# Kernel optimization log

Measured on AMD Instinct MI355X. Metric: run time of the kernel, lower is better.

Reference implementation:

```python
import jax, jax.numpy as jnp
import numpy as np

D, T, F, H = 5, 8192, 768, 64


def setup_inputs() -> dict:
    key = jax.random.key(0)
    ks = jax.random.split(key, 30)
    s = 0.05
    rn = lambda k, shape: jax.random.normal(k, shape, dtype=jnp.float32) * s
    return {
        "text_input": jax.random.normal(ks[0], (1, D, T, F), dtype=jnp.float32),
        "time_inputs": jax.random.uniform(ks[1], (1, D, T), dtype=jnp.float32),
        "num_layer": 0,
        # TimeLSTM params (PyTorch Linear convention: W [out,in], y = x @ W.T + b)
        "W_all_w": rn(ks[2], (4 * H, H)), "W_all_b": rn(ks[3], (4 * H,)),
        "U_all_w": rn(ks[4], (4 * H, F)), "U_all_b": rn(ks[5], (4 * H,)),
        "W_d_w": rn(ks[6], (H, H)), "W_d_b": rn(ks[7], (H,)),
        # text attention
        "ta_W1_w": rn(ks[8], (H, H)), "ta_W1_b": rn(ks[9], (H,)),
        "ta_W2_w": rn(ks[10], (H, H)), "ta_W2_b": rn(ks[11], (H,)),
        "ta_V_w": rn(ks[12], (1, H)), "ta_V_b": rn(ks[13], (1,)),
        # day nn.LSTM(64,64) params, gate order i,f,g,o
        "lstm_Wih": rn(ks[14], (4 * H, H)), "lstm_Whh": rn(ks[15], (4 * H, H)),
        "lstm_bih": rn(ks[16], (4 * H,)), "lstm_bhh": rn(ks[17], (4 * H,)),
        # day attention
        "da_W1_w": rn(ks[18], (H, H)), "da_W1_b": rn(ks[19], (H,)),
        "da_W2_w": rn(ks[20], (H, H)), "da_W2_b": rn(ks[21], (H,)),
        "da_V_w": rn(ks[22], (1, H)), "da_V_b": rn(ks[23], (1,)),
        "stock_w": rn(ks[24], (1, H)), "stock_b": rn(ks[25], (1,)),
    }


def reference(text_input, time_inputs, num_layer,
              W_all_w, W_all_b, U_all_w, U_all_b, W_d_w, W_d_b,
              ta_W1_w, ta_W1_b, ta_W2_w, ta_W2_b, ta_V_w, ta_V_b,
              lstm_Wih, lstm_Whh, lstm_bih, lstm_bhh,
              da_W1_w, da_W1_b, da_W2_w, da_W2_b, da_V_w, da_V_b,
              stock_w, stock_b):
    x = text_input[0]      # [D, T, F] -- days are independent, vectorize over them
    ts = time_inputs[0]    # [D, T]
    d = x.shape[0]

    # Precompute the big input projection as one GEMM: [D,T,4H]
    ux = jnp.einsum('dtf,gf->dtg', x, U_all_w) + U_all_b
    ux_t = jnp.transpose(ux, (1, 0, 2))  # [T, D, 4H]
    ts_t = ts.T                          # [T, D]

    def step(carry, inp):
        h, c = carry
        u, t = inp
        c_s1 = jnp.tanh(c @ W_d_w.T + W_d_b)
        c_adj = c - c_s1 + c_s1 * t[:, None]
        outs = h @ W_all_w.T + W_all_b + u
        f, i, o, g = jnp.split(outs, 4, axis=1)  # TimeLSTM chunk order f,i,o,c_tmp
        f = jax.nn.sigmoid(f); i = jax.nn.sigmoid(i); o = jax.nn.sigmoid(o)
        c = f * c_adj + i * jnp.tanh(g)
        h = o * jnp.tanh(c)
        return (h, c), o  # original appends the (sigmoided) output gate

    h0 = jnp.zeros((d, H), x.dtype)
    (h_fin, _), outs = jax.lax.scan(step, (h0, h0), (ux_t, ts_t))
    y = jnp.tanh(jnp.transpose(outs, (1, 0, 2)))  # [D, T, H]

    # text attention: additive attention pooled over T, per day
    score = jnp.tanh((h_fin @ ta_W1_w.T + ta_W1_b)[:, None, :] + y @ ta_W2_w.T + ta_W2_b) @ ta_V_w.T + ta_V_b
    attn = jax.nn.softmax(score, axis=1)          # [D, T, 1]
    ctx = jnp.sum(attn * y, axis=1)               # [D, H]

    # day nn.LSTM: input [1, D, 64] is (seq=1, batch=D) -> a single LSTM step per day
    h0d = jnp.zeros_like(ctx)
    gates = ctx @ lstm_Wih.T + lstm_bih + h0d @ lstm_Whh.T + lstm_bhh
    gi, gf, gg, go = jnp.split(gates, 4, axis=1)  # PyTorch gate order i,f,g,o
    c_d = jax.nn.sigmoid(gi) * jnp.tanh(gg)       # c0 = 0 so forget path vanishes
    h_d = jax.nn.sigmoid(go) * jnp.tanh(c_d)      # [D, H]

    full = jnp.tanh(h_d)[None]                    # tanh(lstm output), [1, D, H]
    last = h_d[None]                              # h_n (no tanh), [1, D, H]
    score2 = jnp.tanh(last @ da_W1_w.T + da_W1_b + full @ da_W2_w.T + da_W2_b) @ da_V_w.T + da_V_b
    attn2 = jax.nn.softmax(score2, axis=1)
    ft = jnp.sum(attn2 * full, axis=1)            # [1, H]

    return 3.0 * jnp.tanh(ft @ stock_w.T + stock_b)  # [1, 1]
```

## Files before the change

kernel.cpp:

```cpp
#include <hip/hip_runtime.h>
#include <hip/hip_bf16.h>
#include <cstdint>

#define DDAYS 5
#define TT 8192
#define FF 768
#define HH 64
#define GG 256

__device__ __forceinline__ float fast_tanh(float x) {
    return 1.f - 2.f / (__expf(2.f * x) + 1.f);
}
__device__ __forceinline__ float fast_sig(float x) {
    return 1.f / (1.f + __expf(-x));
}

__global__ __launch_bounds__(256, 2) void gemm_ux(
    const float* __restrict__ A, const float* __restrict__ B,
    float* __restrict__ C)
{
    __shared__ __align__(16) float As[16][132];
    __shared__ __align__(16) float Bs[16][132];
    const int tid = threadIdx.x;
    const int m0 = blockIdx.x * 128;
    const int n0 = blockIdx.y * 128;
    const int tx = tid & 15, ty = tid >> 4;
    const int i0 = tx * 8, j0 = ty * 8;
    const int lrow = tid >> 2, lc4 = tid & 3;

    const float* Ap = A + (size_t)(m0 + lrow) * FF + lc4 * 4;
    const float* Bp = B + (size_t)(n0 + lrow) * FF + lc4 * 4;

    float4 pa0 = *(const float4*)(Ap);
    float4 pa1 = *(const float4*)(Ap + 64 * FF);
    float4 pb0 = *(const float4*)(Bp);
    float4 pb1 = *(const float4*)(Bp + 64 * FF);

    float acc[8][8] = {};

    for (int kt = 0; kt < FF / 16; ++kt) {
        __syncthreads();
        {
            const int kk = lc4 * 4;
            As[kk + 0][lrow] = pa0.x; As[kk + 1][lrow] = pa0.y;
            As[kk + 2][lrow] = pa0.z; As[kk + 3][lrow] = pa0.w;
            As[kk + 0][lrow + 64] = pa1.x; As[kk + 1][lrow + 64] = pa1.y;
            As[kk + 2][lrow + 64] = pa1.z; As[kk + 3][lrow + 64] = pa1.w;
            Bs[kk + 0][lrow] = pb0.x; Bs[kk + 1][lrow] = pb0.y;
            Bs[kk + 2][lrow] = pb0.z; Bs[kk + 3][lrow] = pb0.w;
            Bs[kk + 0][lrow + 64] = pb1.x; Bs[kk + 1][lrow + 64] = pb1.y;
            Bs[kk + 2][lrow + 64] = pb1.z; Bs[kk + 3][lrow + 64] = pb1.w;
        }
        __syncthreads();
        if (kt + 1 < FF / 16) {
            const int k0 = (kt + 1) * 16;
            pa0 = *(const float4*)(Ap + k0);
            pa1 = *(const float4*)(Ap + 64 * FF + k0);
            pb0 = *(const float4*)(Bp + k0);
            pb1 = *(const float4*)(Bp + 64 * FF + k0);
        }
#pragma unroll
        for (int k = 0; k < 16; ++k) {
            float a[8], b[8];
            *(float4*)&a[0] = *(const float4*)&As[k][i0];
            *(float4*)&a[4] = *(const float4*)&As[k][i0 + 4];
            *(float4*)&b[0] = *(const float4*)&Bs[k][j0];
            *(float4*)&b[4] = *(const float4*)&Bs[k][j0 + 4];
#pragma unroll
            for (int r = 0; r < 8; ++r)
#pragma unroll
                for (int c = 0; c < 8; ++c)
                    acc[r][c] = fmaf(a[r], b[c], acc[r][c]);
        }
    }
#pragma unroll
    for (int r = 0; r < 8; ++r) {
        float4 s0 = make_float4(acc[r][0], acc[r][1], acc[r][2], acc[r][3]);
        float4 s1 = make_float4(acc[r][4], acc[r][5], acc[r][6], acc[r][7]);
        float* Cp = C + (size_t)(m0 + i0 + r) * GG + n0 + j0;
        *(float4*)Cp = s0;
        *(float4*)(Cp + 4) = s1;
    }
}

__global__ __launch_bounds__(256, 1) void scan_kernel(
    const float* __restrict__ ux, const float* __restrict__ ts,
    const float* __restrict__ Ww, const float* __restrict__ Wb,
    const float* __restrict__ Ub,
    const float* __restrict__ Dw, const float* __restrict__ Db,
    float* __restrict__ y, float* __restrict__ hfin)
{
    const int d = blockIdx.x;
    const int tid = threadIdx.x;
    const int wv = tid >> 6;
    const int lane = tid & 63;
    const int gt = lane >> 4;
    const int jl = lane & 15;
    const int jj = (wv << 4) | jl;
    const int row = (gt << 6) | jj;

    float wall[64];
#pragma unroll
    for (int k = 0; k < 16; k++) {
        float4 v = *(const float4*)&Ww[row * 64 + 4 * k];
        wall[4 * k] = v.x; wall[4 * k + 1] = v.y;
        wall[4 * k + 2] = v.z; wall[4 * k + 3] = v.w;
    }
    const float bias = Wb[row] + Ub[row];

    float wd16[16];
#pragma unroll
    for (int k = 0; k < 4; k++) {
        float4 v = *(const float4*)&Dw[jj * 64 + gt * 16 + 4 * k];
        wd16[4 * k] = v.x; wd16[4 * k + 1] = v.y;
        wd16[4 * k + 2] = v.z; wd16[4 * k + 3] = v.w;
    }
    const float wdb = Db[jj];

    __shared__ __align__(16) float h_all[2][64];
    __shared__ __align__(16) float c_all[2][64];
    if (tid < 64) { h_all[0][tid] = 0.f; c_all[0][tid] = 0.f; }
    __syncthreads();

    const float* uxd = ux + (size_t)d * TT * GG + row;
    const float* tsd = ts + (size_t)d * TT;
    float* yd = y + (size_t)d * TT * HH;

    float up[4], tp[4];
#pragma unroll
    for (int i = 0; i < 4; i++) {
        up[i] = uxd[(size_t)i * GG];
        tp[i] = tsd[i];
    }

    for (int t = 0; t < TT; t += 4) {
#pragma unroll
        for (int i = 0; i < 4; ++i) {
            const int tc = t + i;
            const int rb = tc & 1, nb = rb ^ 1;
            const float ucur = up[i], tcur = tp[i];
            {
                int tn = tc + 4; if (tn > TT - 1) tn = TT - 1;
                up[i] = uxd[(size_t)tn * GG];
                tp[i] = tsd[tn];
            }

            float a0 = 0.f, a1 = 0.f, a2 = 0.f, a3 = 0.f;
#pragma unroll
            for (int k = 0; k < 64; k += 4) {
                float4 h4 = *(const float4*)&h_all[rb][k];
                a0 = fmaf(h4.x, wall[k], a0);
                a1 = fmaf(h4.y, wall[k + 1], a1);
                a2 = fmaf(h4.z, wall[k + 2], a2);
                a3 = fmaf(h4.w, wall[k + 3], a3);
            }
            float p0 = 0.f, p1 = 0.f;
#pragma unroll
            for (int k = 0; k < 16; k += 4) {
                float4 c4 = *(const float4*)&c_all[rb][(gt << 4) + k];
                p0 = fmaf(c4.x, wd16[k], p0);
                p1 = fmaf(c4.y, wd16[k + 1], p1);
                p0 = fmaf(c4.z, wd16[k + 2], p0);
                p1 = fmaf(c4.w, wd16[k + 3], p1);
            }
            float p = p0 + p1;
            p += __shfl_xor(p, 16);
            p += __shfl_xor(p, 32);
            const float cs1 = fast_tanh(p + wdb);

            const float pre = (a0 + a1) + (a2 + a3) + bias + ucur;
            const float gv = (gt == 3) ? fast_tanh(pre) : fast_sig(pre);

            const float c_old = c_all[rb][jj];

            const float fg = __shfl(gv, jl);
            const float ig = __shfl(gv, jl + 16);
            const float og = __shfl(gv, jl + 32);
            const float gg = __shfl(gv, jl + 48);

            const float cadj = c_old + cs1 * (tcur - 1.f);
            const float cn = fmaf(fg, cadj, ig * gg);
            const float hn = og * fast_tanh(cn);

            if (gt == 2) yd[(size_t)tc * HH + jj] = fast_tanh(gv);
            if (gt == 0) { h_all[nb][jj] = hn; c_all[nb][jj] = cn; }

            asm volatile("s_waitcnt lgkmcnt(0)" ::: "memory");
            __builtin_amdgcn_sched_barrier(0);
            __builtin_amdgcn_s_barrier();
            __builtin_amdgcn_sched_barrier(0);
        }
    }
    if (tid < 64) hfin[d * 64 + tid] = h_all[0][tid];
}

#define TW 32
__global__ __launch_bounds__(256) void score_kernel(
    const float* __restrict__ y, const float* __restrict__ hfin,
    const float* __restrict__ W1, const float* __restrict__ b1,
    const float* __restrict__ W2, const float* __restrict__ b2,
    const float* __restrict__ Vw, const float* __restrict__ Vb,
    float* __restrict__ score)
{
    const int d = blockIdx.y;
    const int tid = threadIdx.x;
    const int lane = tid & 63, wv = tid >> 6;
    __shared__ __align__(16) float hf[64];
    __shared__ float qs[64];
    if (tid < 64) hf[tid] = hfin[d * 64 + tid];
    __syncthreads();
    if (tid < 64) {
        float acc = b1[tid];
#pragma unroll
        for (int k = 0; k < 16; k++) {
            float4 w = *(const float4*)&W1[tid * 64 + 4 * k];
            float4 h4 = *(const float4*)&hf[4 * k];
            acc += w.x * h4.x + w.y * h4.y + w.z * h4.z + w.w * h4.w;
        }
        qs[tid] = acc;
    }
    __syncthreads();

    float w2[64];
#pragma unroll
    for (int k = 0; k < 16; k++) {
        float4 v = *(const float4*)&W2[lane * 64 + 4 * k];
        w2[4 * k] = v.x; w2[4 * k + 1] = v.y;
        w2[4 * k + 2] = v.z; w2[4 * k + 3] = v.w;
    }
    const float qb = qs[lane] + b2[lane];
    const float vr = Vw[lane];
    const float vb = Vb[0];
    const int tbase = blockIdx.x * (4 * TW) + wv * TW;
    const float* yd = y + (size_t)d * TT * HH;

    for (int i = 0; i < TW; i++) {
        const int t = tbase + i;
        const float* yrow = yd + (size_t)t * HH;
        float a0 = 0.f, a1 = 0.f, a2 = 0.f, a3 = 0.f;
#pragma unroll
        for (int k = 0; k < 64; k += 4) {
            float4 yv = *(const float4*)&yrow[k];
            a0 = fmaf(yv.x, w2[k], a0);
            a1 = fmaf(yv.y, w2[k + 1], a1);
            a2 = fmaf(yv.z, w2[k + 2], a2);
            a3 = fmaf(yv.w, w2[k + 3], a3);
        }
        float v = fast_tanh(qb + (a0 + a1) + (a2 + a3));
        float s = v * vr;
#pragma unroll
        for (int off = 32; off > 0; off >>= 1) s += __shfl_xor(s, off);
        if (lane == 0) score[(size_t)d * TT + t] = s + vb;
    }
}

__global__ __launch_bounds__(256) void ctx_kernel(
    const float* __restrict__ score, const float* __restrict__ y,
    float* __restrict__ ctx)
{
    const int d = blockIdx.x;
    const int tid = threadIdx.x;
    __shared__ float red[256];
    const float* sc = score + (size_t)d * TT;

    float m = -1e30f;
    for (int t = tid; t < TT; t += 256) m = fmaxf(m, sc[t]);
    red[tid] = m; __syncthreads();
    for (int s = 128; s > 0; s >>= 1) {
        if (tid < s) red[tid] = fmaxf(red[tid], red[tid + s]);
        __syncthreads();
    }
    m = red[0]; __syncthreads();

    float se = 0.f;
    for (int t = tid; t < TT; t += 256) se += __expf(sc[t] - m);
    red[tid] = se; __syncthreads();
    for (int s = 128; s > 0; s >>= 1) {
        if (tid < s) red[tid] += red[tid + s];
        __syncthreads();
    }
    const float inv = 1.f / red[0];
    __syncthreads();

    const int j = tid & 63, grp = tid >> 6;
    const float* yd = y + (size_t)d * TT * HH;
    float a = 0.f;
    for (int t = grp; t < TT; t += 4)
        a = fmaf(__expf(sc[t] - m), yd[(size_t)t * HH + j], a);
    red[tid] = a; __syncthreads();
    if (tid < 64)
        ctx[d * 64 + tid] =
            (red[tid] + red[tid + 64] + red[tid + 128] + red[tid + 192]) * inv;
}

__global__ __launch_bounds__(320) void final_kernel(
    const float* __restrict__ ctx,
    const float* __restrict__ Wih, const float* __restrict__ bih,
    const float* __restrict__ bhh,
    const float* __restrict__ W1, const float* __restrict__ b1,
    const float* __restrict__ W2, const float* __restrict__ b2,
    const float* __restrict__ Vw, const float* __restrict__ Vb,
    const float* __restrict__ stw, const float* __restrict__ stb,
    float* __restrict__ out)
{
    const int tid = threadIdx.x;
    const int dd = tid >> 6, j = tid & 63;
    __shared__ __align__(16) float ctxs[320];
    __shared__ float gsh[5 * 256];
    __shared__ __align__(16) float fulls[320];
    __shared__ __align__(16) float lasts[320];
    __shared__ float s2[5];

    ctxs[tid] = ctx[tid];
    __syncthreads();

    if (tid < 256) {
        float w[64];
#pragma unroll
        for (int k = 0; k < 16; k++) {
            float4 v = *(const float4*)&Wih[tid * 64 + 4 * k];
            w[4 * k] = v.x; w[4 * k + 1] = v.y;
            w[4 * k + 2] = v.z; w[4 * k + 3] = v.w;
        }
        const float bb = bih[tid] + bhh[tid];
        for (int dday = 0; dday < 5; ++dday) {
            float acc = bb;
#pragma unroll
            for (int k = 0; k < 64; k += 4) {
                float4 c4 = *(const float4*)&ctxs[dday * 64 + k];
                acc += w[k] * c4.x + w[k + 1] * c4.y + w[k + 2] * c4.z +
                       w[k + 3] * c4.w;
            }
            gsh[dday * 256 + tid] = acc;
        }
    }
    __syncthreads();
    {
        float gi = gsh[dd * 256 + j];
        float gg2 = gsh[dd * 256 + 128 + j];
        float go = gsh[dd * 256 + 192 + j];
        float c = fast_sig(gi) * fast_tanh(gg2);
        float hd = fast_sig(go) * fast_tanh(c);
        lasts[tid] = hd;
        fulls[tid] = fast_tanh(hd);
    }
    __syncthreads();
    {
        float w1r[64], w2r[64];
#pragma unroll
        for (int k = 0; k < 16; k++) {
            float4 v1 = *(const float4*)&W1[j * 64 + 4 * k];
            float4 v2 = *(const float4*)&W2[j * 64 + 4 * k];
            w1r[4 * k] = v1.x; w1r[4 * k + 1] = v1.y;
            w1r[4 * k + 2] = v1.z; w1r[4 * k + 3] = v1.w;
            w2r[4 * k] = v2.x; w2r[4 * k + 1] = v2.y;
            w2r[4 * k + 2] = v2.z; w2r[4 * k + 3] = v2.w;
        }
        float acc = b1[j] + b2[j];
#pragma unroll
        for (int k = 0; k < 64; ++k)
            acc += w1r[k] * lasts[dd * 64 + k] + w2r[k] * fulls[dd * 64 + k];
        float v = fast_tanh(acc) * Vw[j];
#pragma unroll
        for (int off = 32; off > 0; off >>= 1) v += __shfl_xor(v, off);
        if (j == 0) s2[dd] = v + Vb[0];
    }
    __syncthreads();
    if (tid < 64) {
        float m = s2[0];
#pragma unroll
        for (int dday = 1; dday < 5; ++dday) m = fmaxf(m, s2[dday]);
        float se = 0.f, ft = 0.f;
#pragma unroll
        for (int dday = 0; dday < 5; ++dday) {
            float e = __expf(s2[dday] - m);
            se += e;
            ft += e * fulls[dday * 64 + tid];
        }
        ft /= se;
        float pv = ft * stw[tid];
#pragma unroll
        for (int off = 32; off > 0; off >>= 1) pv += __shfl_xor(pv, off);
        if (tid == 0) out[0] = 3.f * fast_tanh(pv + stb[0]);
    }
}

extern "C" void kernel_launch(void* const* d_in, const int* in_sizes, int n_in,
                              void* d_out, int out_size, void* d_ws,
                              size_t ws_size, hipStream_t stream)
{
    const float* x     = (const float*)d_in[0];
    const float* ts    = (const float*)d_in[1];
    const float* Wallw = (const float*)d_in[3];
    const float* Wallb = (const float*)d_in[4];
    const float* Uallw = (const float*)d_in[5];
    const float* Uallb = (const float*)d_in[6];
    const float* Wdw   = (const float*)d_in[7];
    const float* Wdb   = (const float*)d_in[8];
    const float* taW1w = (const float*)d_in[9];
    const float* taW1b = (const float*)d_in[10];
    const float* taW2w = (const float*)d_in[11];
    const float* taW2b = (const float*)d_in[12];
    const float* taVw  = (const float*)d_in[13];
    const float* taVb  = (const float*)d_in[14];
    const float* Wih   = (const float*)d_in[15];
    const float* bih   = (const float*)d_in[17];
    const float* bhh   = (const float*)d_in[18];
    const float* daW1w = (const float*)d_in[19];
    const float* daW1b = (const float*)d_in[20];
    const float* daW2w = (const float*)d_in[21];
    const float* daW2b = (const float*)d_in[22];
    const float* daVw  = (const float*)d_in[23];
    const float* daVb  = (const float*)d_in[24];
    const float* stw   = (const float*)d_in[25];
    const float* stb   = (const float*)d_in[26];
    float* out = (float*)d_out;

    float* ux = (float*)d_ws;
    float* yb = ux + (size_t)DDAYS * TT * GG;
    float* sc = yb + (size_t)DDAYS * TT * HH;
    float* hf = sc + (size_t)DDAYS * TT;
    float* cx = hf + 512;

    gemm_ux<<<dim3(320, 2), 256, 0, stream>>>(x, Uallw, ux);
    scan_kernel<<<dim3(DDAYS), 256, 0, stream>>>(ux, ts, Wallw, Wallb, Uallb,
                                                 Wdw, Wdb, yb, hf);
    score_kernel<<<dim3(TT / (4 * TW), DDAYS), 256, 0, stream>>>(
        yb, hf, taW1w, taW1b, taW2w, taW2b, taVw, taVb, sc);
    ctx_kernel<<<dim3(DDAYS), 256, 0, stream>>>(sc, yb, cx);
    final_kernel<<<dim3(1), 320, 0, stream>>>(cx, Wih, bih, bhh, daW1w, daW1b,
                                              daW2w, daW2b, daVw, daVb, stw,
                                              stb, out);
}
```

Baseline: 6.824 ms.

## Halve scan block to two waves with fp16 dot2 recurrent matvec

Restructures the serial TimeLSTM scan so each thread computes two gate rows, which lets the block shrink from four waves to two and cuts barrier cost per timestep. Recurrent and decay weights plus the h/c state exchanged through LDS are stored as fp16 and reduced with packed dot2 instructions. The tanh gate is computed through a scaled sigmoid so all lanes follow the same path, and c is kept in registers. The costs are reduced precision in the 8192-step recurrence, which may let error accumulate, and more work per thread.

```diff
diff --git a/kernel.cpp b/kernel.cpp
--- a/kernel.cpp
+++ b/kernel.cpp
@@ -7,6 +7,14 @@
 #define FF 768
 #define HH 64
 #define GG 256
+
+typedef _Float16 h2f __attribute__((ext_vector_type(2)));
+
+#if __has_builtin(__builtin_amdgcn_fdot2)
+#define FDOT2(a, b, c) __builtin_amdgcn_fdot2((a), (b), (c), false)
+#else
+#define FDOT2(a, b, c) fmaf((float)(a).x, (float)(b).x, fmaf((float)(a).y, (float)(b).y, (c)))
+#endif
 
 __device__ __forceinline__ float fast_tanh(float x) {
     return 1.f - 2.f / (__expf(2.f * x) + 1.f);
@@ -83,7 +91,7 @@
     }
 }
 
-__global__ __launch_bounds__(256, 1) void scan_kernel(
+__global__ __launch_bounds__(128, 1) void scan_kernel(
     const float* __restrict__ ux, const float* __restrict__ ts,
     const float* __restrict__ Ww, const float* __restrict__ Wb,
     const float* __restrict__ Ub,
@@ -93,97 +101,145 @@
     const int d = blockIdx.x;
     const int tid = threadIdx.x;
     const int wv = tid >> 6;
-    const int lane = tid & 63;
-    const int gt = lane >> 4;
-    const int jl = lane & 15;
-    const int jj = (wv << 4) | jl;
-    const int row = (gt << 6) | jj;
-
-    float wall[64];
-#pragma unroll
-    for (int k = 0; k < 16; k++) {
-        float4 v = *(const float4*)&Ww[row * 64 + 4 * k];
-        wall[4 * k] = v.x; wall[4 * k + 1] = v.y;
-        wall[4 * k + 2] = v.z; wall[4 * k + 3] = v.w;
-    }
-    const float bias = Wb[row] + Ub[row];
-
-    float wd16[16];
-#pragma unroll
-    for (int k = 0; k < 4; k++) {
-        float4 v = *(const float4*)&Dw[jj * 64 + gt * 16 + 4 * k];
-        wd16[4 * k] = v.x; wd16[4 * k + 1] = v.y;
-        wd16[4 * k + 2] = v.z; wd16[4 * k + 3] = v.w;
-    }
+    const int l  = tid & 63;
+    const int jl = l & 31;
+    const int g0 = l >> 5;
+    const int jj = (wv << 5) | jl;
+    const int rA = (g0 << 6) + jj;
+    const int rB = 128 + (g0 << 6) + jj;
+
+    h2f wAr[32], wBr[32], wdr[16];
+    {
+        const float2* pA = (const float2*)(Ww + (size_t)rA * 64);
+        const float2* pB = (const float2*)(Ww + (size_t)rB * 64);
+#pragma unroll
+        for (int k = 0; k < 32; ++k) {
+            float2 a = pA[k], b = pB[k];
+            wAr[k] = h2f{(_Float16)a.x, (_Float16)a.y};
+            wBr[k] = h2f{(_Float16)b.x, (_Float16)b.y};
+        }
+        const float2* pD = (const float2*)(Dw + (size_t)jj * 64 + (g0 << 5));
+#pragma unroll
+        for (int k = 0; k < 16; ++k) {
+            float2 v = pD[k];
+            wdr[k] = h2f{(_Float16)v.x, (_Float16)v.y};
+        }
+    }
+    const float biasA = Wb[rA] + Ub[rA];
+    const float biasB = Wb[rB] + Ub[rB];
     const float wdb = Db[jj];
-
-    __shared__ __align__(16) float h_all[2][64];
-    __shared__ __align__(16) float c_all[2][64];
-    if (tid < 64) { h_all[0][tid] = 0.f; c_all[0][tid] = 0.f; }
-    __syncthreads();
-
-    const float* uxd = ux + (size_t)d * TT * GG + row;
-    const float* tsd = ts + (size_t)d * TT;
+    const float bmul = g0 ? 2.f : 1.f;
+    const float bsub = g0 ? 1.f : 0.f;
+
+    __shared__ __align__(16) _Float16 h_lds[2][64];
+    __shared__ __align__(16) _Float16 c_lds[2][64];
+    if (tid < 64) {
+        h_lds[0][tid] = (_Float16)0.f;
+        c_lds[0][tid] = (_Float16)0.f;
+    }
+    __syncthreads();
+
+    const float* uxd  = ux + (size_t)d * TT * GG;
+    const float* uA_p = uxd + rA;
+    const float* uB_p = uxd + rB;
+    const float* tsd  = ts + (size_t)d * TT;
     float* yd = y + (size_t)d * TT * HH;
 
-    float up[4], tp[4];
-#pragma unroll
-    for (int i = 0; i < 4; i++) {
-        up[i] = uxd[(size_t)i * GG];
+    float uA[4], uB[4], tp[4];
+#pragma unroll
+    for (int i = 0; i < 4; ++i) {
+        uA[i] = uA_p[(size_t)i * GG];
+        uB[i] = uB_p[(size_t)i * GG];
         tp[i] = tsd[i];
     }
+
+    float c_old = 0.f;
 
     for (int t = 0; t < TT; t += 4) {
 #pragma unroll
         for (int i = 0; i < 4; ++i) {
             const int tc = t + i;
             const int rb = tc & 1, nb = rb ^ 1;
-            const float ucur = up[i], tcur = tp[i];
+            const float ucA = uA[i], ucB = uB[i], tcur = tp[i];
             {
                 int tn = tc + 4; if (tn > TT - 1) tn = TT - 1;
-                up[i] = uxd[(size_t)tn * GG];
+                uA[i] = uA_p[(size_t)tn * GG];
+                uB[i] = uB_p[(size_t)tn * GG];
                 tp[i] = tsd[tn];
             }
 
+            h2f hp[32];
+            {
+                const uint4* hb = (const uint4*)&h_lds[rb][0];
+#pragma unroll
+                for (int k = 0; k < 8; ++k) {
+                    uint4 v = hb[k];
+                    hp[4 * k + 0] = __builtin_bit_cast(h2f, v.x);
+                    hp[4 * k + 1] = __builtin_bit_cast(h2f, v.y);
+                    hp[4 * k + 2] = __builtin_bit_cast(h2f, v.z);
+                    hp[4 * k + 3] = __builtin_bit_cast(h2f, v.w);
+                }
+            }
+            h2f cp[16];
+            {
+                const uint4* cb = (const uint4*)(&c_lds[rb][0] + (g0 << 5));
+#pragma unroll
+                for (int k = 0; k < 4; ++k) {
+                    uint4 v = cb[k];
+                    cp[4 * k + 0] = __builtin_bit_cast(h2f, v.x);
+                    cp[4 * k + 1] = __builtin_bit_cast(h2f, v.y);
+                    cp[4 * k + 2] = __builtin_bit_cast(h2f, v.z);
+                    cp[4 * k + 3] = __builtin_bit_cast(h2f, v.w);
+                }
+            }
+
             float a0 = 0.f, a1 = 0.f, a2 = 0.f, a3 = 0.f;
-#pragma unroll
-            for (int k = 0; k < 64; k += 4) {
-                float4 h4 = *(const float4*)&h_all[rb][k];
-                a0 = fmaf(h4.x, wall[k], a0);
-                a1 = fmaf(h4.y, wall[k + 1], a1);
-                a2 = fmaf(h4.z, wall[k + 2], a2);
-                a3 = fmaf(h4.w, wall[k + 3], a3);
+            float b0 = 0.f, b1 = 0.f, b2 = 0.f, b3 = 0.f;
+#pragma unroll
+            for (int k = 0; k < 32; k += 4) {
+                a0 = FDOT2(wAr[k + 0], hp[k + 0], a0);
+                a1 = FDOT2(wAr[k + 1], hp[k + 1], a1);
+                a2 = FDOT2(wAr[k + 2], hp[k + 2], a2);
+                a3 = FDOT2(wAr[k + 3], hp[k + 3], a3);
+                b0 = FDOT2(wBr[k + 0], hp[k + 0], b0);
+                b1 = FDOT2(wBr[k + 1], hp[k + 1], b1);
+                b2 = FDOT2(wBr[k + 2], hp[k + 2], b2);
+                b3 = FDOT2(wBr[k + 3], hp[k + 3], b3);
             }
             float p0 = 0.f, p1 = 0.f;
 #pragma unroll
-            for (int k = 0; k < 16; k += 4) {
-                float4 c4 = *(const float4*)&c_all[rb][(gt << 4) + k];
-                p0 = fmaf(c4.x, wd16[k], p0);
-                p1 = fmaf(c4.y, wd16[k + 1], p1);
-                p0 = fmaf(c4.z, wd16[k + 2], p0);
-                p1 = fmaf(c4.w, wd16[k + 3], p1);
+            for (int k = 0; k < 16; k += 2) {
+                p0 = FDOT2(wdr[k + 0], cp[k + 0], p0);
+                p1 = FDOT2(wdr[k + 1], cp[k + 1], p1);
             }
             float p = p0 + p1;
-            p += __shfl_xor(p, 16);
             p += __shfl_xor(p, 32);
             const float cs1 = fast_tanh(p + wdb);
 
-            const float pre = (a0 + a1) + (a2 + a3) + bias + ucur;
-            const float gv = (gt == 3) ? fast_tanh(pre) : fast_sig(pre);
-
-            const float c_old = c_all[rb][jj];
-
-            const float fg = __shfl(gv, jl);
-            const float ig = __shfl(gv, jl + 16);
-            const float og = __shfl(gv, jl + 32);
-            const float gg = __shfl(gv, jl + 48);
-
-            const float cadj = c_old + cs1 * (tcur - 1.f);
-            const float cn = fmaf(fg, cadj, ig * gg);
-            const float hn = og * fast_tanh(cn);
-
-            if (gt == 2) yd[(size_t)tc * HH + jj] = fast_tanh(gv);
-            if (gt == 0) { h_all[nb][jj] = hn; c_all[nb][jj] = cn; }
+            const float preA = (a0 + a1) + (a2 + a3) + biasA + ucA;
+            const float preB = (b0 + b1) + (b2 + b3) + biasB + ucB;
+            const float gA = fast_sig(preA);
+            const float q  = fast_sig(preB * bmul);
+            const float gB = fmaf(q, bmul, -bsub);
+
+            const float gA2 = __shfl_xor(gA, 32);
+            const float gB2 = __shfl_xor(gB, 32);
+            const float f  = g0 ? gA2 : gA;
+            const float ii = g0 ? gA  : gA2;
+            const float oo = g0 ? gB2 : gB;
+            const float gg = g0 ? gB  : gB2;
+
+            const float cadj = fmaf(cs1, tcur - 1.f, c_old);
+            const float cn = fmaf(f, cadj, ii * gg);
+            const float hn = oo * fast_tanh(cn);
+            c_old = cn;
+
+            if (g0 == 0) {
+                h_lds[nb][jj] = (_Float16)hn;
+                yd[(size_t)tc * HH + jj] = fast_tanh(gB);
+            } else {
+                c_lds[nb][jj] = (_Float16)cn;
+            }
 
             asm volatile("s_waitcnt lgkmcnt(0)" ::: "memory");
             __builtin_amdgcn_sched_barrier(0);
@@ -191,7 +247,7 @@
             __builtin_amdgcn_sched_barrier(0);
         }
     }
-    if (tid < 64) hfin[d * 64 + tid] = h_all[0][tid];
+    if (tid < 64) hfin[d * 64 + tid] = (float)h_lds[0][tid];
 }
 
 #define TW 32
@@ -423,7 +479,7 @@
     float* cx = hf + 512;
 
     gemm_ux<<<dim3(320, 2), 256, 0, stream>>>(x, Uallw, ux);
-    scan_kernel<<<dim3(DDAYS), 256, 0, stream>>>(ux, ts, Wallw, Wallb, Uallb,
+    scan_kernel<<<dim3(DDAYS), 128, 0, stream>>>(ux, ts, Wallw, Wallb, Uallb,
                                                  Wdw, Wdb, yb, hf);
     score_kernel<<<dim3(TT / (4 * TW), DDAYS), 256, 0, stream>>>(
         yb, hf, taW1w, taW1b, taW2w, taW2b, taVw, taVb, sc);
```

Result: faster. 5.510 ms (-19.2%).
